# Kernel optimization log

Hardware: AMD Instinct MI355X
Metric: run time of the kernel (lower is better)

The kernel has to match this reference:

```python
import jax, jax.numpy as jnp
import numpy as np

B, S, H, F, G = 8, 2048, 1024, 4096, 128
EPS = 1e-5


def setup_inputs() -> dict:
    key = jax.random.key(0)
    ks = jax.random.split(key, 8)
    x = jax.random.normal(ks[0], (B, S, H), dtype=jnp.float32)
    ln_gamma = jnp.ones((H,), jnp.float32)
    ln_beta = jnp.zeros((H,), jnp.float32)
    # int8-style quantized weights stored as int32 in [0, 256) with zero-point 128
    fc1_q = jax.random.randint(ks[1], (H, F), 0, 256, dtype=jnp.int32)
    fc2_q = jax.random.randint(ks[2], (F, H), 0, 256, dtype=jnp.int32)
    # per-group scales (one scale per 128 rows of K, per output column)
    fc1_scales = jax.random.uniform(ks[3], (H // G, F), jnp.float32) * 0.02 + 0.001
    fc2_scales = jax.random.uniform(ks[4], (F // G, H), jnp.float32) * 0.02 + 0.001
    fc1_bias = jax.random.normal(ks[5], (F,), jnp.float32) * 0.02
    fc2_bias = jax.random.normal(ks[6], (H,), jnp.float32) * 0.02
    return {"x": x, "ln_gamma": ln_gamma, "ln_beta": ln_beta,
            "fc1_q": fc1_q, "fc1_scales": fc1_scales, "fc1_bias": fc1_bias,
            "fc2_q": fc2_q, "fc2_scales": fc2_scales, "fc2_bias": fc2_bias}


def _dequant(q, scales, g):
    # q: [K, N] int, scales: [K//g, N]; zero-point 128 symmetric int8 scheme
    K, N = q.shape
    w = (q.astype(jnp.float32) - 128.0).reshape(K // g, g, N) * scales[:, None, :]
    return w.reshape(K, N)


def reference(x, ln_gamma, ln_beta, fc1_q, fc1_scales, fc1_bias, fc2_q, fc2_scales, fc2_bias):
    residual = x
    # LayerNorm over last dim
    mu = jnp.mean(x, axis=-1, keepdims=True)
    var = jnp.mean(jnp.square(x - mu), axis=-1, keepdims=True)
    h = (x - mu) * jax.lax.rsqrt(var + EPS) * ln_gamma + ln_beta
    hf = h.reshape(-1, H)                       # [B*S, H]
    w1 = _dequant(fc1_q, fc1_scales, G)         # [H, F]
    y = hf @ w1 + fc1_bias                      # [B*S, F]
    y = jax.nn.silu(y)                          # dropout is identity at inference
    w2 = _dequant(fc2_q, fc2_scales, G)         # [F, H]
    z = y @ w2 + fc2_bias                       # [B*S, H]
    return residual + 0.5 * z.reshape(residual.shape)
```

## Files before the change

kernel.cpp:

```cpp
#include <hip/hip_runtime.h>
#include <hip/hip_bf16.h>

#define HH 1024
#define FF 4096
#define MTOT (8 * 2048)

typedef __attribute__((ext_vector_type(4))) float f32x4;
typedef __attribute__((ext_vector_type(8))) short bf16x8;

__device__ inline void async_load16(const void* g, void* l) {
    __builtin_amdgcn_global_load_lds(
        (const __attribute__((address_space(1))) unsigned int*)g,
        (__attribute__((address_space(3))) unsigned int*)l, 16, 0, 0);
}
__device__ inline unsigned lds_off(void* p) {
    return (unsigned)(size_t)(__attribute__((address_space(3))) char*)p;
}
template<int OFF>
__device__ inline bf16x8 dsr(unsigned addr) {
    bf16x8 r;
    asm volatile("ds_read_b128 %0, %1 offset:%2" : "=v"(r) : "v"(addr), "n"(OFF));
    return r;
}
#define SBAR()  __builtin_amdgcn_s_barrier()
#define LGKM0() do { asm volatile("s_waitcnt lgkmcnt(0)"); \
                     __builtin_amdgcn_sched_barrier(0); } while (0)
#define WAIT_VM0() asm volatile("s_waitcnt vmcnt(0)")

template<int BUF, int MH>
__device__ inline void ldA(bf16x8 (&d)[4][2], unsigned vA0, unsigned vA1) {
    constexpr int B = BUF * 32768 + MH * 8192;
    d[0][0] = dsr<B + 0>(vA0);     d[0][1] = dsr<B + 0>(vA1);
    d[1][0] = dsr<B + 2048>(vA0);  d[1][1] = dsr<B + 2048>(vA1);
    d[2][0] = dsr<B + 4096>(vA0);  d[2][1] = dsr<B + 4096>(vA1);
    d[3][0] = dsr<B + 6144>(vA0);  d[3][1] = dsr<B + 6144>(vA1);
}
template<int BUF, int NH>
__device__ inline void ldB(bf16x8 (&d)[2][2], unsigned vB0, unsigned vB1) {
    constexpr int B = BUF * 32768 + NH * 4096;
    d[0][0] = dsr<B + 0>(vB0);     d[0][1] = dsr<B + 0>(vB1);
    d[1][0] = dsr<B + 2048>(vB0);  d[1][1] = dsr<B + 2048>(vB1);
}

__global__ void dequant_t_kernel(const int* __restrict__ q,
                                 const float* __restrict__ scales,
                                 __hip_bfloat16* __restrict__ wt,
                                 int K, int N)
{
    __shared__ float tile[32][33];
    const int n0 = blockIdx.x * 32, k0 = blockIdx.y * 32;
    const int tx = threadIdx.x, ty = threadIdx.y;
#pragma unroll
    for (int i = 0; i < 32; i += 8) {
        int k = k0 + ty + i, n = n0 + tx;
        float s = scales[(size_t)(k >> 7) * N + n];
        tile[ty + i][tx] = (float)(q[(size_t)k * N + n] - 128) * s;
    }
    __syncthreads();
#pragma unroll
    for (int i = 0; i < 32; i += 8) {
        int n = n0 + ty + i, k = k0 + tx;
        wt[(size_t)n * K + k] = __float2bfloat16(tile[tx][ty + i]);
    }
}

__global__ __launch_bounds__(256)
void ln_kernel(const float* __restrict__ x, const float* __restrict__ gamma,
               const float* __restrict__ beta, __hip_bfloat16* __restrict__ hf,
               int m0)
{
    const int row = m0 + blockIdx.x;
    const float4 v = ((const float4*)(x + (size_t)row * HH))[threadIdx.x];
    float s  = v.x + v.y + v.z + v.w;
    float ss = v.x * v.x + v.y * v.y + v.z * v.z + v.w * v.w;
#pragma unroll
    for (int o = 32; o > 0; o >>= 1) { s += __shfl_down(s, o); ss += __shfl_down(ss, o); }
    __shared__ float red[8];
    const int wid = threadIdx.x >> 6, lane = threadIdx.x & 63;
    if (lane == 0) { red[wid] = s; red[4 + wid] = ss; }
    __syncthreads();
    if (threadIdx.x == 0) {
        red[0] = red[0] + red[1] + red[2] + red[3];
        red[4] = red[4] + red[5] + red[6] + red[7];
    }
    __syncthreads();
    const float mu   = red[0] * (1.f / HH);
    const float rstd = rsqrtf(red[4] * (1.f / HH) - mu * mu + 1e-5f);
    const float4 g = ((const float4*)gamma)[threadIdx.x];
    const float4 b = ((const float4*)beta)[threadIdx.x];
    float h0 = (v.x - mu) * rstd * g.x + b.x;
    float h1 = (v.y - mu) * rstd * g.y + b.y;
    float h2 = (v.z - mu) * rstd * g.z + b.z;
    float h3 = (v.w - mu) * rstd * g.w + b.w;
    __hip_bfloat16 t0 = __float2bfloat16(h0), t1 = __float2bfloat16(h1);
    __hip_bfloat16 t2 = __float2bfloat16(h2), t3 = __float2bfloat16(h3);
    ushort4 o;
    o.x = *(unsigned short*)&t0; o.y = *(unsigned short*)&t1;
    o.z = *(unsigned short*)&t2; o.w = *(unsigned short*)&t3;
    ((ushort4*)(hf + (size_t)blockIdx.x * HH))[threadIdx.x] = o;
}

template<int EPI, int KK>
__global__ __launch_bounds__(512, 2)
void gemm256(const __hip_bfloat16* __restrict__ A,
             const __hip_bfloat16* __restrict__ Bt,
             const float* __restrict__ bias,
             const float* __restrict__ resid,
             void* __restrict__ outv,
             int N, int nbx)
{
    __shared__ __align__(16) short SM[65536];
    constexpr int NT = KK >> 6;

    const int nwg = (int)gridDim.x, b = (int)blockIdx.x;
    const int nby = nwg / nbx;
    int bx, by;
    if (((nwg & 255) == 0) && ((nbx & 3) == 0) && ((nby & 7) == 0)) {
        const int x = b & 7, p = b >> 3;
        const int s = (p >> 5) * 8 + x;
        const int t = p & 31;
        const int sbx = nbx >> 2;
        bx = (s % sbx) * 4 + (t & 3);
        by = (s / sbx) * 8 + (t >> 2);
    } else {
        const int q = nwg >> 3, r = nwg & 7;
        const int xcd = b & 7, pos = b >> 3;
        const int bid = (xcd < r) ? xcd * (q + 1) + pos
                                  : r * (q + 1) + (xcd - r) * q + pos;
        bx = bid % nbx; by = bid / nbx;
    }
    const int rowA0 = by * 256, colB0 = bx * 256;

    const int tid = (int)threadIdx.x;
    const int lane = tid & 63, wid = tid >> 6;
    const int wr = wid >> 2, wc = wid & 3;
    const int lrow = lane & 15, kg = lane >> 4;
    const int swz = lrow & 7;

    const int srow = tid >> 3;
    const int sgs  = (tid & 7) ^ (srow & 7);
    const __hip_bfloat16* aSrc = A  + (size_t)(rowA0 + srow) * KK + sgs * 8;
    const __hip_bfloat16* bSrc = Bt + (size_t)(colB0 + srow) * KK + sgs * 8;
    short* aDst = SM + srow * 64 + (tid & 7) * 8;
    short* bDst = SM + 32768 + srow * 64 + (tid & 7) * 8;

    const unsigned asB = lds_off(SM);
    const unsigned k0off = (unsigned)((kg ^ swz) << 4);
    const unsigned k1off = (unsigned)(((4 + kg) ^ swz) << 4);
    const unsigned vA0 = asB + (unsigned)((wr * 128 + lrow) * 128) + k0off;
    const unsigned vA1 = asB + (unsigned)((wr * 128 + lrow) * 128) + k1off;
    const unsigned vB0 = asB + 65536u + (unsigned)((wc * 64 + lrow) * 128) + k0off;
    const unsigned vB1 = asB + 65536u + (unsigned)((wc * 64 + lrow) * 128) + k1off;

    auto stA = [&](int buf, int t, int half) {
        const size_t ko = (size_t)t * 64;
        short* d = aDst + buf * 16384 + half * 8192;
        const __hip_bfloat16* s0 = aSrc + (size_t)(half * 128) * KK + ko;
        async_load16(s0, d);
        async_load16(s0 + (size_t)64 * KK, d + 4096);
    };
    auto stB = [&](int buf, int t, int half) {
        const size_t ko = (size_t)t * 64;
        short* d = bDst + buf * 16384 + half * 8192;
        const __hip_bfloat16* s0 = bSrc + (size_t)(half * 128) * KK + ko;
        async_load16(s0, d);
        async_load16(s0 + (size_t)64 * KK, d + 4096);
    };

    f32x4 acc[8][4] = {};
    auto mf = [&](const bf16x8 (&a)[4][2], const bf16x8 (&bb)[2][2], int mh, int nh) {
        __builtin_amdgcn_s_setprio(1);
#pragma unroll
        for (int ks = 0; ks < 2; ++ks)
#pragma unroll
            for (int m2 = 0; m2 < 4; ++m2)
#pragma unroll
                for (int n2 = 0; n2 < 2; ++n2)
                    acc[mh * 4 + m2][nh * 2 + n2] =
                        __builtin_amdgcn_mfma_f32_16x16x32_bf16(
                            a[m2][ks], bb[n2][ks], acc[mh * 4 + m2][nh * 2 + n2], 0, 0, 0);
        __builtin_amdgcn_s_setprio(0);
    };

    stA(0, 0, 0); stA(0, 0, 1); stB(0, 0, 0); stB(0, 0, 1);
    WAIT_VM0();
    SBAR();

    bf16x8 a0[4][2], a1[4][2], b0[2][2], b1[2][2];
    const int NI = NT >> 1;
    for (int i = 0; i < NI; ++i) {
        const int c = 2 * i, n = 2 * i + 1;
        stA(1, n, 0); stA(1, n, 1); stB(1, n, 0); stB(1, n, 1);
        ldA<0, 0>(a0, vA0, vA1);
        ldB<0, 0>(b0, vB0, vB1);
        ldB<0, 1>(b1, vB0, vB1);
        ldA<0, 1>(a1, vA0, vA1);
        LGKM0();
        mf(a0, b0, 0, 0);
        mf(a0, b1, 0, 1);
        mf(a1, b0, 1, 0);
        mf(a1, b1, 1, 1);
        WAIT_VM0();
        SBAR();
        if (i < NI - 1) { stA(0, c + 2, 0); stA(0, c + 2, 1);
                          stB(0, c + 2, 0); stB(0, c + 2, 1); }
        ldA<1, 0>(a0, vA0, vA1);
        ldB<1, 0>(b0, vB0, vB1);
        ldB<1, 1>(b1, vB0, vB1);
        ldA<1, 1>(a1, vA0, vA1);
        LGKM0();
        mf(a0, b0, 0, 0);
        mf(a0, b1, 0, 1);
        mf(a1, b0, 1, 0);
        mf(a1, b1, 1, 1);
        WAIT_VM0();
        SBAR();
    }

    __syncthreads();

    if (EPI == 0) {
        short* smh = SM;
#pragma unroll
        for (int ni = 0; ni < 4; ++ni) {
            const int col = wc * 64 + ni * 16 + lrow;
            const float bv = bias[colB0 + col];
#pragma unroll
            for (int mi = 0; mi < 8; ++mi) {
#pragma unroll
                for (int j = 0; j < 4; ++j) {
                    const int rowl = wr * 128 + mi * 16 + kg * 4 + j;
                    const float v = acc[mi][ni][j] + bv;
                    const float sv = v / (1.f + __expf(-v));
                    const __hip_bfloat16 hb = __float2bfloat16(sv);
                    const int sidx = rowl * 256 + ((((col >> 3) ^ (rowl & 7)) << 3) | (col & 7));
                    smh[sidx] = *(const short*)&hb;
                }
            }
        }
        __syncthreads();
        __hip_bfloat16* yp = (__hip_bfloat16*)outv;
#pragma unroll
        for (int p = 0; p < 16; ++p) {
            const int idx = p * 512 + tid;
            const int rowl = idx >> 5, s = idx & 31;
            const bf16x8 v8 = *(const bf16x8*)&smh[rowl * 256 + ((s ^ (rowl & 7)) << 3)];
            *(bf16x8*)(yp + (size_t)(rowA0 + rowl) * N + colB0 + s * 8) = v8;
        }
    } else {
        float* smf = (float*)SM;
        float* op = (float*)outv;
#pragma unroll
        for (int h = 0; h < 2; ++h) {
            if (wr == h) {
#pragma unroll
                for (int ni = 0; ni < 4; ++ni) {
                    const int col = wc * 64 + ni * 16 + lrow;
                    const float bv = bias[colB0 + col];
#pragma unroll
                    for (int mi = 0; mi < 8; ++mi) {
#pragma unroll
                        for (int j = 0; j < 4; ++j) {
                            const int rowl = mi * 16 + kg * 4 + j;
                            const float v = acc[mi][ni][j] + bv;
                            const int fidx = rowl * 256 +
                                ((((col >> 2) ^ (rowl & 7)) << 2) | (col & 3));
                            smf[fidx] = v;
                        }
                    }
                }
            }
            __syncthreads();
#pragma unroll
            for (int p = 0; p < 16; ++p) {
                const int idx = p * 512 + tid;
                const int rowl = idx >> 6, s = idx & 63;
                const f32x4 v4 = *(const f32x4*)&smf[rowl * 256 + ((s ^ (rowl & 7)) << 2)];
                const size_t g = (size_t)(rowA0 + h * 128 + rowl) * N + colB0 + s * 4;
                const float4 rv = *(const float4*)&resid[g];
                float4 o4;
                o4.x = rv.x + 0.5f * v4[0];
                o4.y = rv.y + 0.5f * v4[1];
                o4.z = rv.z + 0.5f * v4[2];
                o4.w = rv.w + 0.5f * v4[3];
                *(float4*)&op[g] = o4;
            }
            __syncthreads();
        }
    }
}

extern "C" void kernel_launch(void* const* d_in, const int* in_sizes, int n_in,
                              void* d_out, int out_size, void* d_ws, size_t ws_size,
                              hipStream_t stream)
{
    const float* x      = (const float*)d_in[0];
    const float* gamma  = (const float*)d_in[1];
    const float* beta   = (const float*)d_in[2];
    const int*   fc1_q  = (const int*)d_in[3];
    const float* fc1_s  = (const float*)d_in[4];
    const float* fc1_b  = (const float*)d_in[5];
    const int*   fc2_q  = (const int*)d_in[6];
    const float* fc2_s  = (const float*)d_in[7];
    const float* fc2_b  = (const float*)d_in[8];
    float* out = (float*)d_out;

    char* ws = (char*)d_ws;
    __hip_bfloat16* w1t = (__hip_bfloat16*)ws;
    __hip_bfloat16* w2t = (__hip_bfloat16*)(ws + (size_t)FF * HH * 2);
    char* dyn = ws + (size_t)2 * FF * HH * 2;
    const size_t avail = ws_size - (size_t)2 * FF * HH * 2;

    int MC = (int)(avail / ((size_t)(HH + FF) * 2));
    MC = (MC / 256) * 256;
    if (MC > MTOT) MC = MTOT;
    if (MC < 256)  MC = 256;

    __hip_bfloat16* hf_c = (__hip_bfloat16*)dyn;
    __hip_bfloat16* y_c  = (__hip_bfloat16*)(dyn + (size_t)MC * HH * 2);

    dequant_t_kernel<<<dim3(FF / 32, HH / 32), dim3(32, 8), 0, stream>>>(
        fc1_q, fc1_s, w1t, HH, FF);
    dequant_t_kernel<<<dim3(HH / 32, FF / 32), dim3(32, 8), 0, stream>>>(
        fc2_q, fc2_s, w2t, FF, HH);

    for (int m0 = 0; m0 < MTOT; m0 += MC) {
        const int mc = (MTOT - m0 < MC) ? (MTOT - m0) : MC;
        ln_kernel<<<mc, 256, 0, stream>>>(x, gamma, beta, hf_c, m0);
        gemm256<0, HH><<<dim3((FF / 256) * (mc / 256)), 512, 0, stream>>>(
            hf_c, w1t, fc1_b, nullptr, (void*)y_c, FF, FF / 256);
        gemm256<1, FF><<<dim3((HH / 256) * (mc / 256)), 512, 0, stream>>>(
            y_c, w2t, fc2_b, x + (size_t)m0 * HH, (void*)(out + (size_t)m0 * HH),
            HH, HH / 256);
    }
}
```

Measured before the change: 312.9 us.

## Switch GEMM mainloop to three-stage BK=32 ring with partial waits

Replaces the two-buffer BK=64 pipeline with a three-stage ring of BK=32 tiles. Each iteration waits only for the oldest stage (vmcnt(4)), so the next prefetch stays in flight across the barrier. LDS fragment reads are split, with MFMAs on the first half of A issued after a partial lgkmcnt wait. It removes the XOR swizzle, which can add LDS bank conflicts, and doubles the number of barriers per K.

After: 324.3 us. 1.04x slower.

```diff
diff --git a/kernel.cpp b/kernel.cpp
--- a/kernel.cpp
+++ b/kernel.cpp
@@ -7,6 +7,8 @@
 
 typedef __attribute__((ext_vector_type(4))) float f32x4;
 typedef __attribute__((ext_vector_type(8))) short bf16x8;
+
+template<int I> struct IC { static constexpr int value = I; };
 
 __device__ inline void async_load16(const void* g, void* l) {
     __builtin_amdgcn_global_load_lds(
@@ -23,23 +25,27 @@
     return r;
 }
 #define SBAR()  __builtin_amdgcn_s_barrier()
-#define LGKM0() do { asm volatile("s_waitcnt lgkmcnt(0)"); \
-                     __builtin_amdgcn_sched_barrier(0); } while (0)
+template<int N>
+__device__ inline void LGKM() {
+    asm volatile("s_waitcnt lgkmcnt(%0)" :: "n"(N));
+    __builtin_amdgcn_sched_barrier(0);
+}
+#define WAIT_VM4() asm volatile("s_waitcnt vmcnt(4)")
 #define WAIT_VM0() asm volatile("s_waitcnt vmcnt(0)")
 
-template<int BUF, int MH>
-__device__ inline void ldA(bf16x8 (&d)[4][2], unsigned vA0, unsigned vA1) {
-    constexpr int B = BUF * 32768 + MH * 8192;
-    d[0][0] = dsr<B + 0>(vA0);     d[0][1] = dsr<B + 0>(vA1);
-    d[1][0] = dsr<B + 2048>(vA0);  d[1][1] = dsr<B + 2048>(vA1);
-    d[2][0] = dsr<B + 4096>(vA0);  d[2][1] = dsr<B + 4096>(vA1);
-    d[3][0] = dsr<B + 6144>(vA0);  d[3][1] = dsr<B + 6144>(vA1);
-}
-template<int BUF, int NH>
-__device__ inline void ldB(bf16x8 (&d)[2][2], unsigned vB0, unsigned vB1) {
-    constexpr int B = BUF * 32768 + NH * 4096;
-    d[0][0] = dsr<B + 0>(vB0);     d[0][1] = dsr<B + 0>(vB1);
-    d[1][0] = dsr<B + 2048>(vB0);  d[1][1] = dsr<B + 2048>(vB1);
+template<int B>
+__device__ inline void ldA8(bf16x8 (&d)[8], unsigned vA) {
+    constexpr int O = B * 16384;
+    d[0] = dsr<O + 0>(vA);    d[1] = dsr<O + 1024>(vA);
+    d[2] = dsr<O + 2048>(vA); d[3] = dsr<O + 3072>(vA);
+    d[4] = dsr<O + 4096>(vA); d[5] = dsr<O + 5120>(vA);
+    d[6] = dsr<O + 6144>(vA); d[7] = dsr<O + 7168>(vA);
+}
+template<int B>
+__device__ inline void ldB4(bf16x8 (&d)[4], unsigned vB) {
+    constexpr int O = B * 16384;
+    d[0] = dsr<O + 0>(vB);    d[1] = dsr<O + 1024>(vB);
+    d[2] = dsr<O + 2048>(vB); d[3] = dsr<O + 3072>(vB);
 }
 
 __global__ void dequant_t_kernel(const int* __restrict__ q,
@@ -110,7 +116,7 @@
              int N, int nbx)
 {
     __shared__ __align__(16) short SM[65536];
-    constexpr int NT = KK >> 6;
+    constexpr int NT = KK >> 5;
 
     const int nwg = (int)gridDim.x, b = (int)blockIdx.x;
     const int nby = nwg / nbx;
@@ -135,87 +141,73 @@
     const int lane = tid & 63, wid = tid >> 6;
     const int wr = wid >> 2, wc = wid & 3;
     const int lrow = lane & 15, kg = lane >> 4;
-    const int swz = lrow & 7;
-
-    const int srow = tid >> 3;
-    const int sgs  = (tid & 7) ^ (srow & 7);
-    const __hip_bfloat16* aSrc = A  + (size_t)(rowA0 + srow) * KK + sgs * 8;
-    const __hip_bfloat16* bSrc = Bt + (size_t)(colB0 + srow) * KK + sgs * 8;
-    short* aDst = SM + srow * 64 + (tid & 7) * 8;
-    short* bDst = SM + 32768 + srow * 64 + (tid & 7) * 8;
+
+    const int srow = tid >> 2;
+    const __hip_bfloat16* aSrc = A  + (size_t)(rowA0 + srow) * KK + (tid & 3) * 8;
+    const __hip_bfloat16* bSrc = Bt + (size_t)(colB0 + srow) * KK + (tid & 3) * 8;
+    short* aDst = SM + srow * 32 + (tid & 3) * 8;
+    short* bDst = SM + 24576 + srow * 32 + (tid & 3) * 8;
 
     const unsigned asB = lds_off(SM);
-    const unsigned k0off = (unsigned)((kg ^ swz) << 4);
-    const unsigned k1off = (unsigned)(((4 + kg) ^ swz) << 4);
-    const unsigned vA0 = asB + (unsigned)((wr * 128 + lrow) * 128) + k0off;
-    const unsigned vA1 = asB + (unsigned)((wr * 128 + lrow) * 128) + k1off;
-    const unsigned vB0 = asB + 65536u + (unsigned)((wc * 64 + lrow) * 128) + k0off;
-    const unsigned vB1 = asB + 65536u + (unsigned)((wc * 64 + lrow) * 128) + k1off;
-
-    auto stA = [&](int buf, int t, int half) {
-        const size_t ko = (size_t)t * 64;
-        short* d = aDst + buf * 16384 + half * 8192;
-        const __hip_bfloat16* s0 = aSrc + (size_t)(half * 128) * KK + ko;
-        async_load16(s0, d);
-        async_load16(s0 + (size_t)64 * KK, d + 4096);
+    const unsigned vA = asB + (unsigned)((wr * 128 + lrow) * 64 + (kg << 4));
+    const unsigned vB = asB + 49152u + (unsigned)((wc * 64 + lrow) * 64 + (kg << 4));
+
+    auto stage = [&](int sb, int t) {
+        const __hip_bfloat16* sA = aSrc + (size_t)t * 32;
+        short* dA = aDst + sb * 8192;
+        async_load16(sA, dA);
+        async_load16(sA + (size_t)128 * KK, dA + 4096);
+        const __hip_bfloat16* sB = bSrc + (size_t)t * 32;
+        short* dB = bDst + sb * 8192;
+        async_load16(sB, dB);
+        async_load16(sB + (size_t)128 * KK, dB + 4096);
     };
-    auto stB = [&](int buf, int t, int half) {
-        const size_t ko = (size_t)t * 64;
-        short* d = bDst + buf * 16384 + half * 8192;
-        const __hip_bfloat16* s0 = bSrc + (size_t)(half * 128) * KK + ko;
-        async_load16(s0, d);
-        async_load16(s0 + (size_t)64 * KK, d + 4096);
+
+    f32x4 acc[8][4] = {};
+
+    auto phase = [&](auto bc, int tstage) {
+        constexpr int B = decltype(bc)::value;
+        const bool st = (tstage < NT);
+        if (st) stage((B + 2) % 3, tstage);
+        bf16x8 a[8], bbf[4];
+        ldB4<B>(bbf, vB);
+        ldA8<B>(a, vA);
+        LGKM<4>();
+        __builtin_amdgcn_s_setprio(1);
+#pragma unroll
+        for (int mi = 0; mi < 4; ++mi)
+#pragma unroll
+            for (int ni = 0; ni < 4; ++ni)
+                acc[mi][ni] = __builtin_amdgcn_mfma_f32_16x16x32_bf16(
+                    a[mi], bbf[ni], acc[mi][ni], 0, 0, 0);
+        __builtin_amdgcn_s_setprio(0);
+        LGKM<0>();
+        __builtin_amdgcn_s_setprio(1);
+#pragma unroll
+        for (int mi = 4; mi < 8; ++mi)
+#pragma unroll
+            for (int ni = 0; ni < 4; ++ni)
+                acc[mi][ni] = __builtin_amdgcn_mfma_f32_16x16x32_bf16(
+                    a[mi], bbf[ni], acc[mi][ni], 0, 0, 0);
+        __builtin_amdgcn_s_setprio(0);
+        if (st) WAIT_VM4();
+        else    WAIT_VM0();
+        SBAR();
     };
 
-    f32x4 acc[8][4] = {};
-    auto mf = [&](const bf16x8 (&a)[4][2], const bf16x8 (&bb)[2][2], int mh, int nh) {
-        __builtin_amdgcn_s_setprio(1);
-#pragma unroll
-        for (int ks = 0; ks < 2; ++ks)
-#pragma unroll
-            for (int m2 = 0; m2 < 4; ++m2)
-#pragma unroll
-                for (int n2 = 0; n2 < 2; ++n2)
-                    acc[mh * 4 + m2][nh * 2 + n2] =
-                        __builtin_amdgcn_mfma_f32_16x16x32_bf16(
-                            a[m2][ks], bb[n2][ks], acc[mh * 4 + m2][nh * 2 + n2], 0, 0, 0);
-        __builtin_amdgcn_s_setprio(0);
-    };
-
-    stA(0, 0, 0); stA(0, 0, 1); stB(0, 0, 0); stB(0, 0, 1);
+    stage(0, 0); stage(1, 1);
+    WAIT_VM4();
+    SBAR();
+
+    int t = 2, p = 0;
+    for (; p + 3 <= NT; p += 3) {
+        phase(IC<0>{}, t); ++t;
+        phase(IC<1>{}, t); ++t;
+        phase(IC<2>{}, t); ++t;
+    }
+    if (p < NT) { phase(IC<0>{}, t); ++t; ++p; }
+    if (p < NT) { phase(IC<1>{}, t); ++t; ++p; }
     WAIT_VM0();
-    SBAR();
-
-    bf16x8 a0[4][2], a1[4][2], b0[2][2], b1[2][2];
-    const int NI = NT >> 1;
-    for (int i = 0; i < NI; ++i) {
-        const int c = 2 * i, n = 2 * i + 1;
-        stA(1, n, 0); stA(1, n, 1); stB(1, n, 0); stB(1, n, 1);
-        ldA<0, 0>(a0, vA0, vA1);
-        ldB<0, 0>(b0, vB0, vB1);
-        ldB<0, 1>(b1, vB0, vB1);
-        ldA<0, 1>(a1, vA0, vA1);
-        LGKM0();
-        mf(a0, b0, 0, 0);
-        mf(a0, b1, 0, 1);
-        mf(a1, b0, 1, 0);
-        mf(a1, b1, 1, 1);
-        WAIT_VM0();
-        SBAR();
-        if (i < NI - 1) { stA(0, c + 2, 0); stA(0, c + 2, 1);
-                          stB(0, c + 2, 0); stB(0, c + 2, 1); }
-        ldA<1, 0>(a0, vA0, vA1);
-        ldB<1, 0>(b0, vB0, vB1);
-        ldB<1, 1>(b1, vB0, vB1);
-        ldA<1, 1>(a1, vA0, vA1);
-        LGKM0();
-        mf(a0, b0, 0, 0);
-        mf(a0, b1, 0, 1);
-        mf(a1, b0, 1, 0);
-        mf(a1, b1, 1, 1);
-        WAIT_VM0();
-        SBAR();
-    }
 
     __syncthreads();
 
@@ -241,8 +233,8 @@
         __syncthreads();
         __hip_bfloat16* yp = (__hip_bfloat16*)outv;
 #pragma unroll
-        for (int p = 0; p < 16; ++p) {
-            const int idx = p * 512 + tid;
+        for (int p2 = 0; p2 < 16; ++p2) {
+            const int idx = p2 * 512 + tid;
             const int rowl = idx >> 5, s = idx & 31;
             const bf16x8 v8 = *(const bf16x8*)&smh[rowl * 256 + ((s ^ (rowl & 7)) << 3)];
             *(bf16x8*)(yp + (size_t)(rowA0 + rowl) * N + colB0 + s * 8) = v8;
@@ -272,8 +264,8 @@
             }
             __syncthreads();
 #pragma unroll
-            for (int p = 0; p < 16; ++p) {
-                const int idx = p * 512 + tid;
+            for (int p2 = 0; p2 < 16; ++p2) {
+                const int idx = p2 * 512 + tid;
                 const int rowl = idx >> 6, s = idx & 63;
                 const f32x4 v4 = *(const f32x4*)&smf[rowl * 256 + ((s ^ (rowl & 7)) << 2)];
                 const size_t g = (size_t)(rowA0 + h * 128 + rowl) * N + colB0 + s * 4;
```
